# Kernel tuning notes

Measured on AMD Instinct MI355X. Metric: run time of the kernel, lower is better.

Reference implementation:

```python
import jax, jax.numpy as jnp
import numpy as np

INPUT_DIM = 1024
EMBED_DIM = 1024
NUM_HEADS = 16
HEAD_DIM = EMBED_DIM // NUM_HEADS


def _xavier_uniform(key, shape):
    fan_in, fan_out = shape[1], shape[0]
    limit = float(np.sqrt(6.0 / (fan_in + fan_out)))
    return jax.random.uniform(key, shape, jnp.float32, -limit, limit)


def setup_inputs() -> dict:
    key = jax.random.key(0)
    kx, kqkv, ko = jax.random.split(key, 3)
    x = jax.random.normal(kx, (2, 2048, INPUT_DIM), jnp.float32)
    # torch Linear stores weight as [out, in]; we keep that convention
    w_qkv = _xavier_uniform(kqkv, (3 * EMBED_DIM, INPUT_DIM))
    b_qkv = jnp.zeros((3 * EMBED_DIM,), jnp.float32)
    w_o = _xavier_uniform(ko, (EMBED_DIM, EMBED_DIM))
    b_o = jnp.zeros((EMBED_DIM,), jnp.float32)
    return {"x": x, "w_qkv": w_qkv, "b_qkv": b_qkv, "w_o": w_o, "b_o": b_o}


def reference(x, w_qkv, b_qkv, w_o, b_o):
    B, S, _ = x.shape
    H, D = NUM_HEADS, HEAD_DIM
    qkv = jnp.einsum("bsi,oi->bso", x, w_qkv) + b_qkv          # [B,S,3E]
    qkv = qkv.reshape(B, S, H, 3 * D).transpose(0, 2, 1, 3)    # [B,H,S,3D]
    q, k, v = jnp.split(qkv, 3, axis=-1)                        # each [B,H,S,D]
    scores = jnp.einsum("bhqd,bhkd->bhqk", q, k) / jnp.sqrt(jnp.float32(D))
    attn = jax.nn.softmax(scores, axis=-1)                      # [B,H,S,S]
    vals = jnp.einsum("bhqk,bhkd->bhqd", attn, v)               # [B,H,S,D]
    vals = vals.transpose(0, 2, 1, 3).reshape(B, S, H * D)      # [B,S,E]
    return jnp.einsum("bse,oe->bso", vals, w_o) + b_o
```

## Files before the change

### kernel.cpp

```cpp
#include <hip/hip_runtime.h>
#include <hip/hip_bf16.h>


typedef __attribute__((ext_vector_type(8))) short bf16x8;
typedef __attribute__((ext_vector_type(4))) short bf16x4;
typedef __attribute__((ext_vector_type(4))) float f32x4;

#define MFMA16(a, b, c) __builtin_amdgcn_mfma_f32_16x16x32_bf16((a), (b), (c), 0, 0, 0)

#if __has_builtin(__builtin_amdgcn_exp2f)
#define EXP2F(x) __builtin_amdgcn_exp2f(x)
#else
#define EXP2F(x) exp2f(x)
#endif

static __device__ __forceinline__ unsigned short f2bf_bits(float v) {
    __hip_bfloat16 h = __float2bfloat16(v);
    return *reinterpret_cast<unsigned short*>(&h);
}

static __device__ __forceinline__ bf16x8 cvt8(const float* p) {
    const f32x4 a = reinterpret_cast<const f32x4*>(p)[0];
    const f32x4 b = reinterpret_cast<const f32x4*>(p)[1];
    bf16x8 r;
    r[0] = (short)f2bf_bits(a[0]); r[1] = (short)f2bf_bits(a[1]);
    r[2] = (short)f2bf_bits(a[2]); r[3] = (short)f2bf_bits(a[3]);
    r[4] = (short)f2bf_bits(b[0]); r[5] = (short)f2bf_bits(b[1]);
    r[6] = (short)f2bf_bits(b[2]); r[7] = (short)f2bf_bits(b[3]);
    return r;
}

__device__ __forceinline__ bf16x8 ldg8(const __hip_bfloat16* p) {
    return *reinterpret_cast<const bf16x8*>(p);
}

__device__ __forceinline__ void load16_lds(const __hip_bfloat16* g, unsigned short* l) {
    __builtin_amdgcn_global_load_lds(
        (const __attribute__((address_space(1))) void*)g,
        (__attribute__((address_space(3))) void*)l, 16, 0, 0);
}

__global__ __launch_bounds__(256)
void cast2_f32_bf16(const float* __restrict__ x, __hip_bfloat16* __restrict__ xb,
                    const float* __restrict__ w, __hip_bfloat16* __restrict__ wb) {
    const int bid = blockIdx.x;
    const float* src = (bid < 512) ? x : w;
    __hip_bfloat16* dst = (bid < 512) ? xb : wb;
    const int rb = (bid < 512) ? bid : (bid - 512);
    const size_t base = (size_t)rb * 8192 + (size_t)threadIdx.x * 32;
#pragma unroll
    for (int i = 0; i < 4; ++i)
        *reinterpret_cast<bf16x8*>(dst + base + i * 8) = cvt8(src + base + i * 8);
}

__global__ __launch_bounds__(256)
void cast_f32_bf16(const float* __restrict__ src, __hip_bfloat16* __restrict__ dst) {
    const size_t base = ((size_t)blockIdx.x * 256 + threadIdx.x) * 32;
#pragma unroll
    for (int i = 0; i < 4; ++i)
        *reinterpret_cast<bf16x8*>(dst + base + i * 8) = cvt8(src + base + i * 8);
}

__global__ __launch_bounds__(256)
void qkv_gemm(const __hip_bfloat16* __restrict__ xb,
              const __hip_bfloat16* __restrict__ wb,
              const float* __restrict__ bqkv,
              __hip_bfloat16* __restrict__ Q,
              __hip_bfloat16* __restrict__ K,
              __hip_bfloat16* __restrict__ Vt) {
    __shared__ unsigned short As[2][128 * 32];
    __shared__ unsigned short Bs[2][128 * 32];

    const int tid  = threadIdx.x;
    const int lane = tid & 63;
    const int wv   = tid >> 6;
    const int quad = lane >> 4;
    const int l16  = lane & 15;
    const int wm   = wv >> 1;
    const int wn   = wv & 1;

    const int bid = blockIdx.x;
    const int xcd = bid & 7;
    const int r   = bid >> 3;
    const int m0  = (r / 3) * 128;
    const int n0  = (xcd * 3 + (r % 3)) * 128;

    const __hip_bfloat16* agl = xb + (size_t)(m0 + wv * 32 + (lane >> 2)) * 1024 + (lane & 3) * 8;
    const __hip_bfloat16* bgl = wb + (size_t)(n0 + wv * 32 + (lane >> 2)) * 1024 + (lane & 3) * 8;

    f32x4 zv = {0.f, 0.f, 0.f, 0.f};
    f32x4 acc[4][4];
#pragma unroll
    for (int ii = 0; ii < 4; ++ii)
#pragma unroll
        for (int jj = 0; jj < 4; ++jj) acc[ii][jj] = zv;

    load16_lds(agl, &As[0][(wv * 32) * 32]);
    load16_lds(agl + 16 * 1024, &As[0][(wv * 32 + 16) * 32]);
    load16_lds(bgl, &Bs[0][(wv * 32) * 32]);
    load16_lds(bgl + 16 * 1024, &Bs[0][(wv * 32 + 16) * 32]);
    __syncthreads();

    for (int k0 = 0; k0 < 1024; k0 += 32) {
        const int p = (k0 >> 5) & 1;
        if (k0 + 32 < 1024) {
            const int q = p ^ 1;
            load16_lds(agl + k0 + 32, &As[q][(wv * 32) * 32]);
            load16_lds(agl + 16 * 1024 + k0 + 32, &As[q][(wv * 32 + 16) * 32]);
            load16_lds(bgl + k0 + 32, &Bs[q][(wv * 32) * 32]);
            load16_lds(bgl + 16 * 1024 + k0 + 32, &Bs[q][(wv * 32 + 16) * 32]);
        }
        bf16x8 af[4], bf[4];
#pragma unroll
        for (int ii = 0; ii < 4; ++ii)
            af[ii] = *reinterpret_cast<const bf16x8*>(
                &As[p][(wm * 64 + ii * 16 + l16) * 32 + quad * 8]);
#pragma unroll
        for (int jj = 0; jj < 4; ++jj)
            bf[jj] = *reinterpret_cast<const bf16x8*>(
                &Bs[p][(wn * 64 + jj * 16 + l16) * 32 + quad * 8]);
#pragma unroll
        for (int ii = 0; ii < 4; ++ii)
#pragma unroll
            for (int jj = 0; jj < 4; ++jj)
                acc[ii][jj] = MFMA16(af[ii], bf[jj], acc[ii][jj]);
        __syncthreads();
    }

    const float QSCALE = 0.18033688011f;

#pragma unroll
    for (int jj = 0; jj < 4; ++jj) {
        const int n = n0 + wn * 64 + jj * 16 + l16;
        const float bias = bqkv[n];
        const int h = n / 192;
        const int r2 = n - h * 192;
        const int t = r2 >> 6;
        const int d = r2 & 63;
#pragma unroll
        for (int ii = 0; ii < 4; ++ii) {
            const int mb = m0 + wm * 64 + ii * 16 + quad * 4;
            const int b = mb >> 11;
            const int s0 = mb & 2047;
            const int bh = b * 16 + h;
            if (t == 2) {
                bf16x4 pk;
#pragma unroll
                for (int i = 0; i < 4; ++i)
                    pk[i] = (short)f2bf_bits(acc[ii][jj][i] + bias);
                *reinterpret_cast<bf16x4*>(&Vt[((size_t)bh * 64 + d) * 2048 + s0]) = pk;
            } else {
#pragma unroll
                for (int i = 0; i < 4; ++i) {
                    const float v = acc[ii][jj][i] + bias;
                    if (t == 0)
                        Q[((size_t)bh * 2048 + s0 + i) * 64 + d] = __float2bfloat16(v * QSCALE);
                    else
                        K[((size_t)bh * 2048 + s0 + i) * 64 + d] = __float2bfloat16(v);
                }
            }
        }
    }
}

__global__ __launch_bounds__(256, 4)
void attn_kernel(const __hip_bfloat16* __restrict__ Q,
                 const __hip_bfloat16* __restrict__ K,
                 const __hip_bfloat16* __restrict__ Vt,
                 __hip_bfloat16* __restrict__ AO) {
    __shared__ unsigned short SB[2][4096];

    const int tid  = threadIdx.x;
    const int lane = tid & 63;
    const int wv   = tid >> 6;
    const int quad = lane >> 4;
    const int l16  = lane & 15;

    const int blk = blockIdx.x;
    const int xcd = blk & 7;
    const int sub = blk >> 3;
    const int bh  = xcd * 4 + (sub & 3);
    const int qb  = sub >> 2;
    const int q0  = qb * 128 + wv * 32;
    const int b   = bh >> 4;
    const int h   = bh & 15;

    const __hip_bfloat16* Qp = Q  + (size_t)bh * 131072;
    const __hip_bfloat16* Kp = K  + (size_t)bh * 131072;
    const __hip_bfloat16* Vp = Vt + (size_t)bh * 131072;

    bf16x8 bQ[2][2];
#pragma unroll
    for (int t = 0; t < 2; ++t)
#pragma unroll
        for (int dh = 0; dh < 2; ++dh)
            bQ[t][dh] = ldg8(Qp + (size_t)(q0 + t * 16 + l16) * 64 + dh * 32 + quad * 8);

    const int kf   = wv;
    const int keyg = (l16 >> 2) * 8 + (l16 & 3) + ((kf >> 1) << 2);
    const int kd0  = (kf & 1) * 32 + quad * 8;
    const __hip_bfloat16* ksrc = Kp + (size_t)keyg * 64 + kd0;
    const __hip_bfloat16* vsrc = Vp + (size_t)(wv * 16 + l16) * 2048 + quad * 8;

    unsigned short* kd[2] = { &SB[0][tid * 8],        &SB[1][tid * 8] };
    unsigned short* vd[2] = { &SB[0][tid * 8 + 2048], &SB[1][tid * 8 + 2048] };

    f32x4 zv = {0.f, 0.f, 0.f, 0.f};
    f32x4 Of[2][4];
#pragma unroll
    for (int t = 0; t < 2; ++t)
#pragma unroll
        for (int jj = 0; jj < 4; ++jj) Of[t][jj] = zv;
    float li[2] = {0.f, 0.f};

    bf16x8 gk = ldg8(ksrc);
    bf16x8 gv = ldg8(vsrc);
    *reinterpret_cast<bf16x8*>(kd[0]) = gk;
    *reinterpret_cast<bf16x8*>(vd[0]) = gv;
    gk = ldg8(ksrc + 2048);
    gv = ldg8(vsrc + 32);
    __syncthreads();

    for (int kt = 0; kt < 64; ++kt) {
        const int p = kt & 1;
        if (kt < 63) {
            *reinterpret_cast<bf16x8*>(kd[p ^ 1]) = gk;
            *reinterpret_cast<bf16x8*>(vd[p ^ 1]) = gv;
        }
        if (kt < 62) {
            gk = ldg8(ksrc + (size_t)(kt + 2) * 2048);
            gv = ldg8(vsrc + (size_t)(kt + 2) * 32);
        }

        const unsigned short* base = &SB[p][lane * 8];
        const bf16x8 aKA0 = *reinterpret_cast<const bf16x8*>(base + 0 * 512);
        const bf16x8 aKA1 = *reinterpret_cast<const bf16x8*>(base + 1 * 512);
        const bf16x8 aKB0 = *reinterpret_cast<const bf16x8*>(base + 2 * 512);
        const bf16x8 aKB1 = *reinterpret_cast<const bf16x8*>(base + 3 * 512);
        bf16x8 aV[4];
#pragma unroll
        for (int jj = 0; jj < 4; ++jj)
            aV[jj] = *reinterpret_cast<const bf16x8*>(base + (4 + jj) * 512);

        f32x4 sA[2], sB[2];
#pragma unroll
        for (int t = 0; t < 2; ++t) {
            sA[t] = zv; sB[t] = zv;
            sA[t] = MFMA16(aKA0, bQ[t][0], sA[t]);
            sA[t] = MFMA16(aKA1, bQ[t][1], sA[t]);
            sB[t] = MFMA16(aKB0, bQ[t][0], sB[t]);
            sB[t] = MFMA16(aKB1, bQ[t][1], sB[t]);
        }

#pragma unroll
        for (int t = 0; t < 2; ++t) {
            float pA[4], pB[4];
#pragma unroll
            for (int i = 0; i < 4; ++i) {
                pA[i] = EXP2F(sA[t][i]);
                pB[i] = EXP2F(sB[t][i]);
            }
            li[t] += ((pA[0] + pA[1]) + (pA[2] + pA[3]))
                   + ((pB[0] + pB[1]) + (pB[2] + pB[3]));

            bf16x8 bP;
            bP[0] = (short)f2bf_bits(pA[0]); bP[1] = (short)f2bf_bits(pA[1]);
            bP[2] = (short)f2bf_bits(pA[2]); bP[3] = (short)f2bf_bits(pA[3]);
            bP[4] = (short)f2bf_bits(pB[0]); bP[5] = (short)f2bf_bits(pB[1]);
            bP[6] = (short)f2bf_bits(pB[2]); bP[7] = (short)f2bf_bits(pB[3]);

#pragma unroll
            for (int jj = 0; jj < 4; ++jj)
                Of[t][jj] = MFMA16(aV[jj], bP, Of[t][jj]);
        }
        __syncthreads();
    }

#pragma unroll
    for (int t = 0; t < 2; ++t) {
        li[t] += __shfl_xor(li[t], 16);
        li[t] += __shfl_xor(li[t], 32);
    }

#pragma unroll
    for (int t = 0; t < 2; ++t) {
        const float linv = 1.f / li[t];
        const int s = q0 + t * 16 + l16;
        __hip_bfloat16* aop = AO + (((size_t)b * 2048 + s) * 16 + h) * 64;
#pragma unroll
        for (int jj = 0; jj < 4; ++jj) {
            bf16x4 pk;
#pragma unroll
            for (int i = 0; i < 4; ++i)
                pk[i] = (short)f2bf_bits(Of[t][jj][i] * linv);
            *reinterpret_cast<bf16x4*>(aop + jj * 16 + quad * 4) = pk;
        }
    }
}

__global__ __launch_bounds__(256)
void out_gemm(const __hip_bfloat16* __restrict__ A,
              const __hip_bfloat16* __restrict__ wob,
              const float* __restrict__ bo,
              float* __restrict__ out) {
    __shared__ unsigned short As[2][64 * 32];
    __shared__ unsigned short Bs[2][128 * 32];

    const int tid  = threadIdx.x;
    const int lane = tid & 63;
    const int wv   = tid >> 6;
    const int quad = lane >> 4;
    const int l16  = lane & 15;
    const int wm   = wv >> 1;
    const int wn   = wv & 1;

    const int bid = blockIdx.x;
    const int m0  = (bid >> 3) * 64;
    const int n0  = (bid & 7) * 128;

    const __hip_bfloat16* agl = A   + (size_t)(m0 + wv * 16 + (lane >> 2)) * 1024 + (lane & 3) * 8;
    const __hip_bfloat16* bgl = wob + (size_t)(n0 + wv * 32 + (lane >> 2)) * 1024 + (lane & 3) * 8;

    f32x4 zv = {0.f, 0.f, 0.f, 0.f};
    f32x4 acc[2][4];
#pragma unroll
    for (int ii = 0; ii < 2; ++ii)
#pragma unroll
        for (int jj = 0; jj < 4; ++jj) acc[ii][jj] = zv;

    load16_lds(agl, &As[0][(wv * 16) * 32]);
    load16_lds(bgl, &Bs[0][(wv * 32) * 32]);
    load16_lds(bgl + 16 * 1024, &Bs[0][(wv * 32 + 16) * 32]);
    __syncthreads();

    for (int k0 = 0; k0 < 1024; k0 += 32) {
        const int p = (k0 >> 5) & 1;
        if (k0 + 32 < 1024) {
            const int q = p ^ 1;
            load16_lds(agl + k0 + 32, &As[q][(wv * 16) * 32]);
            load16_lds(bgl + k0 + 32, &Bs[q][(wv * 32) * 32]);
            load16_lds(bgl + 16 * 1024 + k0 + 32, &Bs[q][(wv * 32 + 16) * 32]);
        }
        bf16x8 af[2], bf[4];
#pragma unroll
        for (int ii = 0; ii < 2; ++ii)
            af[ii] = *reinterpret_cast<const bf16x8*>(
                &As[p][(wm * 32 + ii * 16 + l16) * 32 + quad * 8]);
#pragma unroll
        for (int jj = 0; jj < 4; ++jj)
            bf[jj] = *reinterpret_cast<const bf16x8*>(
                &Bs[p][(wn * 64 + jj * 16 + l16) * 32 + quad * 8]);
#pragma unroll
        for (int ii = 0; ii < 2; ++ii)
#pragma unroll
            for (int jj = 0; jj < 4; ++jj)
                acc[ii][jj] = MFMA16(af[ii], bf[jj], acc[ii][jj]);
        __syncthreads();
    }

#pragma unroll
    for (int jj = 0; jj < 4; ++jj) {
        const int n = n0 + wn * 64 + jj * 16 + l16;
        const float bias = bo[n];
#pragma unroll
        for (int ii = 0; ii < 2; ++ii) {
#pragma unroll
            for (int i = 0; i < 4; ++i) {
                const int m = m0 + wm * 32 + ii * 16 + quad * 4 + i;
                out[(size_t)m * 1024 + n] = acc[ii][jj][i] + bias;
            }
        }
    }
}

extern "C" void kernel_launch(void* const* d_in, const int* in_sizes, int n_in,
                              void* d_out, int out_size, void* d_ws, size_t ws_size,
                              hipStream_t stream) {
    const float* x    = (const float*)d_in[0];
    const float* wqkv = (const float*)d_in[1];
    const float* bqkv = (const float*)d_in[2];
    const float* wo   = (const float*)d_in[3];
    const float* bo   = (const float*)d_in[4];
    float* out = (float*)d_out;

    __hip_bfloat16* ws = (__hip_bfloat16*)d_ws;
    __hip_bfloat16* Q   = ws;
    __hip_bfloat16* K   = ws + (size_t)4194304;
    __hip_bfloat16* Vt  = ws + (size_t)8388608;
    __hip_bfloat16* AO  = ws + (size_t)12582912;
    __hip_bfloat16* wob = Q;

    __hip_bfloat16* xb     = (__hip_bfloat16*)d_out;
    __hip_bfloat16* wqkvb  = xb + (size_t)4194304;

    cast2_f32_bf16<<<dim3(896), 256, 0, stream>>>(x, xb, wqkv, wqkvb);
    qkv_gemm<<<dim3(768), 256, 0, stream>>>(xb, wqkvb, bqkv, Q, K, Vt);
    attn_kernel<<<dim3(512), 256, 0, stream>>>(Q, K, Vt, AO);
    cast_f32_bf16<<<dim3(128), 256, 0, stream>>>(wo, wob);
    out_gemm<<<dim3(512), 256, 0, stream>>>(AO, wob, bo, out);
}
```

Baseline: 197.4 us.

## Split attention key range across two wave groups per block and merge in LDS

The attention block grows from 256 to 512 threads. Two groups of four waves each process half of the 2048 keys for the same 128 queries, so the serial key loop is half as long and each CU holds more waves. At the end, group 1 writes its partial output accumulators and row sums to shared memory, reusing the K/V staging buffer, and group 0 adds them before normalising and storing. This costs more LDS, an extra block-wide barrier and a combine step, and assumes both halves share the same softmax reference so their partial sums can be added directly.

```diff
diff --git a/kernel.cpp b/kernel.cpp
--- a/kernel.cpp
+++ b/kernel.cpp
@@ -163,16 +163,19 @@
     }
 }
 
-__global__ __launch_bounds__(256, 4)
+__global__ __launch_bounds__(512, 4)
 void attn_kernel(const __hip_bfloat16* __restrict__ Q,
                  const __hip_bfloat16* __restrict__ K,
                  const __hip_bfloat16* __restrict__ Vt,
                  __hip_bfloat16* __restrict__ AO) {
-    __shared__ unsigned short SB[2][4096];
+    __shared__ unsigned short SB[2][2][4096];
+    __shared__ float LiX[4][2][64];
 
     const int tid  = threadIdx.x;
     const int lane = tid & 63;
     const int wv   = tid >> 6;
+    const int grp  = wv >> 2;
+    const int wq   = wv & 3;
     const int quad = lane >> 4;
     const int l16  = lane & 15;
 
@@ -181,9 +184,10 @@
     const int sub = blk >> 3;
     const int bh  = xcd * 4 + (sub & 3);
     const int qb  = sub >> 2;
-    const int q0  = qb * 128 + wv * 32;
+    const int q0  = qb * 128 + wq * 32;
     const int b   = bh >> 4;
     const int h   = bh & 15;
+    const int key0 = grp * 1024;
 
     const __hip_bfloat16* Qp = Q  + (size_t)bh * 131072;
     const __hip_bfloat16* Kp = K  + (size_t)bh * 131072;
@@ -196,14 +200,14 @@
         for (int dh = 0; dh < 2; ++dh)
             bQ[t][dh] = ldg8(Qp + (size_t)(q0 + t * 16 + l16) * 64 + dh * 32 + quad * 8);
 
-    const int kf   = wv;
-    const int keyg = (l16 >> 2) * 8 + (l16 & 3) + ((kf >> 1) << 2);
-    const int kd0  = (kf & 1) * 32 + quad * 8;
-    const __hip_bfloat16* ksrc = Kp + (size_t)keyg * 64 + kd0;
-    const __hip_bfloat16* vsrc = Vp + (size_t)(wv * 16 + l16) * 2048 + quad * 8;
-
-    unsigned short* kd[2] = { &SB[0][tid * 8],        &SB[1][tid * 8] };
-    unsigned short* vd[2] = { &SB[0][tid * 8 + 2048], &SB[1][tid * 8 + 2048] };
+    const int keyg = (l16 >> 2) * 8 + (l16 & 3) + ((wq >> 1) << 2);
+    const int kd0  = (wq & 1) * 32 + quad * 8;
+    const __hip_bfloat16* ksrc = Kp + (size_t)(key0 + keyg) * 64 + kd0;
+    const __hip_bfloat16* vsrc = Vp + (size_t)(wq * 16 + l16) * 2048 + key0 + quad * 8;
+
+    const int gt = wq * 64 + lane;
+    unsigned short* kd[2] = { &SB[grp][0][gt * 8],        &SB[grp][1][gt * 8] };
+    unsigned short* vd[2] = { &SB[grp][0][gt * 8 + 2048], &SB[grp][1][gt * 8 + 2048] };
 
     f32x4 zv = {0.f, 0.f, 0.f, 0.f};
     f32x4 Of[2][4];
@@ -221,18 +225,18 @@
     gv = ldg8(vsrc + 32);
     __syncthreads();
 
-    for (int kt = 0; kt < 64; ++kt) {
+    for (int kt = 0; kt < 32; ++kt) {
         const int p = kt & 1;
-        if (kt < 63) {
+        if (kt < 31) {
             *reinterpret_cast<bf16x8*>(kd[p ^ 1]) = gk;
             *reinterpret_cast<bf16x8*>(vd[p ^ 1]) = gv;
         }
-        if (kt < 62) {
+        if (kt < 30) {
             gk = ldg8(ksrc + (size_t)(kt + 2) * 2048);
             gv = ldg8(vsrc + (size_t)(kt + 2) * 32);
         }
 
-        const unsigned short* base = &SB[p][lane * 8];
+        const unsigned short* base = &SB[grp][p][lane * 8];
         const bf16x8 aKA0 = *reinterpret_cast<const bf16x8*>(base + 0 * 512);
         const bf16x8 aKA1 = *reinterpret_cast<const bf16x8*>(base + 1 * 512);
         const bf16x8 aKB0 = *reinterpret_cast<const bf16x8*>(base + 2 * 512);
@@ -282,18 +286,32 @@
         li[t] += __shfl_xor(li[t], 32);
     }
 
-#pragma unroll
-    for (int t = 0; t < 2; ++t) {
-        const float linv = 1.f / li[t];
-        const int s = q0 + t * 16 + l16;
-        __hip_bfloat16* aop = AO + (((size_t)b * 2048 + s) * 16 + h) * 64;
-#pragma unroll
-        for (int jj = 0; jj < 4; ++jj) {
-            bf16x4 pk;
-#pragma unroll
-            for (int i = 0; i < 4; ++i)
-                pk[i] = (short)f2bf_bits(Of[t][jj][i] * linv);
-            *reinterpret_cast<bf16x4*>(aop + jj * 16 + quad * 4) = pk;
+    f32x4* xf = reinterpret_cast<f32x4*>(&SB[0][0][0]);
+    if (grp == 1) {
+#pragma unroll
+        for (int t = 0; t < 2; ++t) {
+            LiX[wq][t][lane] = li[t];
+#pragma unroll
+            for (int jj = 0; jj < 4; ++jj)
+                xf[wq * 512 + (t * 4 + jj) * 64 + lane] = Of[t][jj];
+        }
+    }
+    __syncthreads();
+    if (grp == 0) {
+#pragma unroll
+        for (int t = 0; t < 2; ++t) {
+            const float linv = 1.f / (li[t] + LiX[wq][t][lane]);
+            const int s = q0 + t * 16 + l16;
+            __hip_bfloat16* aop = AO + (((size_t)b * 2048 + s) * 16 + h) * 64;
+#pragma unroll
+            for (int jj = 0; jj < 4; ++jj) {
+                const f32x4 o2 = xf[wq * 512 + (t * 4 + jj) * 64 + lane];
+                bf16x4 pk;
+#pragma unroll
+                for (int i = 0; i < 4; ++i)
+                    pk[i] = (short)f2bf_bits((Of[t][jj][i] + o2[i]) * linv);
+                *reinterpret_cast<bf16x4*>(aop + jj * 16 + quad * 4) = pk;
+            }
         }
     }
 }
@@ -395,7 +413,7 @@
 
     cast2_f32_bf16<<<dim3(896), 256, 0, stream>>>(x, xb, wqkv, wqkvb);
     qkv_gemm<<<dim3(768), 256, 0, stream>>>(xb, wqkvb, bqkv, Q, K, Vt);
-    attn_kernel<<<dim3(512), 256, 0, stream>>>(Q, K, Vt, AO);
+    attn_kernel<<<dim3(512), 512, 0, stream>>>(Q, K, Vt, AO);
     cast_f32_bf16<<<dim3(128), 256, 0, stream>>>(wo, wob);
     out_gemm<<<dim3(512), 256, 0, stream>>>(AO, wob, bo, out);
 }
```

New measurement: 193.5 us. 1.02x faster.
